# Kernel optimization log

Hardware: AMD Instinct MI355X
Metric: run time of the kernel (lower is better)

The kernel has to match this reference:

```python
import jax, jax.numpy as jnp
import numpy as np

N, FEAT, EMB, OUT = 16384, 256, 128, 128


def setup_inputs() -> dict:
    key = jax.random.key(0)
    k1, k2, k3, k4, k5 = jax.random.split(key, 5)
    s1 = 1.0 / np.sqrt(FEAT)
    s2 = 1.0 / np.sqrt(EMB)
    return {
        "x": jax.random.normal(k1, (N, FEAT), dtype=jnp.float32),
        "W1": jax.random.uniform(k2, (FEAT, EMB), jnp.float32, -s1, s1),
        "b1": jax.random.uniform(k3, (EMB,), jnp.float32, -s1, s1),
        "W2": jax.random.uniform(k4, (EMB, OUT), jnp.float32, -s2, s2),
        "b2": jax.random.uniform(k5, (OUT,), jnp.float32, -s2, s2),
    }


def reference(x, W1, b1, W2, b2):
    # projection: [N, feat] -> [N, emb]
    h = x @ W1 + b1
    # dense self-similarity graph: A_ = h h^T  (N x N)
    A_ = h @ h.T
    # degree-style normalization: A_ij -> 2*A_ij / (A_ii + A_jj)
    d = jnp.diagonal(A_)  # [N], == row squared norms of h
    A = 2.0 * A_ / (d[:, None] + d[None, :])
    # degree-normalized aggregation then output MLP + ReLU
    agg = A @ h  # [N, emb]
    return jax.nn.relu(agg @ W2 + b2)
```

## Files before the change

### kernel.cpp

```cpp
#include <hip/hip_runtime.h>
#include <stdint.h>

#define N_TOK 16384
#define FEAT  256
#define EMB   128
#define NQ    13
#define KC    16

typedef float  f32x4  __attribute__((ext_vector_type(4)));
typedef __bf16 bf16x8 __attribute__((ext_vector_type(8)));
typedef short  s16x8  __attribute__((ext_vector_type(8)));
typedef unsigned int u32x4 __attribute__((ext_vector_type(4)));

__device__ __forceinline__ unsigned short bf16_rne(float f) {
    union { float f; unsigned u; } v; v.f = f;
    unsigned u = v.u;
    return (unsigned short)((u + 0x7FFFu + ((u >> 16) & 1u)) >> 16);
}
__device__ __forceinline__ float bf16_to_f32(unsigned short s) {
    union { unsigned u; float f; } v; v.u = ((unsigned)s) << 16; return v.f;
}
__device__ __forceinline__ unsigned pack_trunc(float a, float b) {
    union { float f; unsigned u; } ua, ub; ua.f = a; ub.f = b;
    return (ub.u & 0xFFFF0000u) | (ua.u >> 16);
}
__device__ __forceinline__ void async_cp16(const void* g, void* l) {
    __builtin_amdgcn_global_load_lds(
        (const __attribute__((address_space(1))) unsigned int*)g,
        (__attribute__((address_space(3))) unsigned int*)l, 16, 0, 0);
}

__global__ void k0_transpose(const float* __restrict__ W1, const float* __restrict__ W2,
                             unsigned short* __restrict__ W1T, unsigned short* __restrict__ W2T)
{
    const int tid  = blockIdx.x * blockDim.x + threadIdx.x;
    const int nthr = gridDim.x * blockDim.x;
    for (int i = tid; i < FEAT * EMB; i += nthr) {
        const int r = i >> 7, c = i & 127;
        W1T[c * FEAT + r] = bf16_rne(W1[i]);
    }
    for (int i = tid; i < EMB * EMB; i += nthr) {
        const int r = i >> 7, c = i & 127;
        W2T[c * EMB + r] = bf16_rne(W2[i]);
    }
}

__global__ __launch_bounds__(256) void k1_proj(
    const float* __restrict__ x, const unsigned short* __restrict__ W1T,
    const float* __restrict__ b1,
    unsigned short* __restrict__ h, unsigned short* __restrict__ hT,
    float* __restrict__ UT)
{
    __shared__ __align__(16) unsigned char W1s[65536];
    __shared__ unsigned short ldsT[128 * 68];
    const int lane = threadIdx.x & 63;
    const int wave = threadIdx.x >> 6;
    const int quad = lane >> 4;
    const int l15  = lane & 15;
    const int arow = blockIdx.x * 64 + wave * 16 + l15;

    float4 xv[16];
    #pragma unroll
    for (int ks = 0; ks < 8; ++ks) {
        const float* xp = x + (size_t)arow * FEAT + ks * 32 + quad * 8;
        xv[2 * ks]     = *(const float4*)xp;
        xv[2 * ks + 1] = *(const float4*)(xp + 4);
    }
    #pragma unroll
    for (int c = 0; c < 16; ++c) {
        const int chunk = wave * 16 + c;
        const int row = chunk * 2 + (lane >> 5);
        const int b = (lane & 31) ^ (row & 15);
        async_cp16(W1T + (size_t)row * FEAT + b * 8, W1s + chunk * 1024);
    }
    bf16x8 afr[8];
    #pragma unroll
    for (int ks = 0; ks < 8; ++ks) {
        const float4 xa = xv[2 * ks], xb = xv[2 * ks + 1];
        s16x8 at;
        at[0] = (short)bf16_rne(xa.x); at[1] = (short)bf16_rne(xa.y);
        at[2] = (short)bf16_rne(xa.z); at[3] = (short)bf16_rne(xa.w);
        at[4] = (short)bf16_rne(xb.x); at[5] = (short)bf16_rne(xb.y);
        at[6] = (short)bf16_rne(xb.z); at[7] = (short)bf16_rne(xb.w);
        afr[ks] = __builtin_bit_cast(bf16x8, at);
    }
    __syncthreads();

    const f32x4 zero4 = {0.f, 0.f, 0.f, 0.f};
    f32x4 acc[8];
    #pragma unroll
    for (int n0 = 0; n0 < 8; ++n0) acc[n0] = zero4;
    #pragma unroll
    for (int ks = 0; ks < 8; ++ks)
        #pragma unroll
        for (int n0 = 0; n0 < 8; ++n0) {
            const int n = n0 * 16 + l15;
            const int b = (ks * 4 + quad) ^ (n & 15);
            const bf16x8 bfr = *(const bf16x8*)(W1s + n * 512 + b * 16);
            acc[n0] = __builtin_amdgcn_mfma_f32_16x16x32_bf16(afr[ks], bfr, acc[n0], 0, 0, 0);
        }

    const int rbase = blockIdx.x * 64 + wave * 16 + quad * 4;
    float dpart[4] = {0.f, 0.f, 0.f, 0.f};
    #pragma unroll
    for (int n0 = 0; n0 < 8; ++n0) {
        const int col = n0 * 16 + l15;
        const float bias = b1[col];
        unsigned short hb[4];
        #pragma unroll
        for (int r = 0; r < 4; ++r) {
            const float hv = acc[n0][r] + bias;
            const unsigned short q = bf16_rne(hv);
            hb[r] = q;
            const float bb = bf16_to_f32(q);
            dpart[r] += bb * bb;
            h[(size_t)(rbase + r) * EMB + col] = q;
        }
        ushort4 pk = make_ushort4(hb[0], hb[1], hb[2], hb[3]);
        *(ushort4*)&ldsT[col * 68 + wave * 16 + quad * 4] = pk;
    }
    const float tql = __expf(0.9f * (float)l15 - 10.8f);
    #pragma unroll
    for (int r = 0; r < 4; ++r) {
        float v = dpart[r];
        v += __shfl_xor(v, 1);
        v += __shfl_xor(v, 2);
        v += __shfl_xor(v, 4);
        v += __shfl_xor(v, 8);
        if (l15 < 12)       UT[(size_t)l15 * N_TOK + rbase + r] = __expf(-tql * v);
        else if (l15 == 12) UT[(size_t)12  * N_TOK + rbase + r] = 1.0f;
    }
    __syncthreads();
    const int rbase0 = blockIdx.x * 64;
    #pragma unroll
    for (int i = 0; i < 4; ++i) {
        const int slot = i * 256 + threadIdx.x;
        const int c    = slot >> 3;
        const int seg  = slot & 7;
        const ushort4 a0 = *(const ushort4*)&ldsT[c * 68 + seg * 8];
        const ushort4 a1 = *(const ushort4*)&ldsT[c * 68 + seg * 8 + 4];
        ushort4 o[2] = {a0, a1};
        *(uint4*)&hT[(size_t)c * N_TOK + rbase0 + seg * 8] = *(const uint4*)o;
    }
}

__global__ __launch_bounds__(256, 3) void k2a_gram(
    const unsigned short* __restrict__ hT, const float* __restrict__ UT,
    float* __restrict__ Gp)
{
    __shared__ __align__(16) unsigned char Rb[32768];
    const int lane = threadIdx.x & 63;
    const int wave = threadIdx.x >> 6;
    const int quad = lane >> 4;
    const int l15  = lane & 15;
    const int q  = blockIdx.x >> 4;
    const int kc = blockIdx.x & 15;
    const int E = wave & 1, F = wave >> 1;

    const f32x4 zero4 = {0.f, 0.f, 0.f, 0.f};
    f32x4 acc[4][4];
    #pragma unroll
    for (int mt = 0; mt < 4; ++mt)
        #pragma unroll
        for (int nt = 0; nt < 4; ++nt) acc[mt][nt] = zero4;

    #pragma unroll 1
    for (int sub = 0; sub < 8; ++sub) {
        const int kwin = kc * 1024 + sub * 128;
        __syncthreads();
        #pragma unroll
        for (int c = 0; c < 8; ++c) {
            const int chunk = wave * 8 + c;
            const int row = chunk * 4 + (lane >> 4);
            const int b = (lane & 15) ^ (row & 15);
            async_cp16(hT + (size_t)row * N_TOK + kwin + b * 8, Rb + chunk * 1024);
        }
        __syncthreads();

        #pragma unroll
        for (int ks = 0; ks < 4; ++ks) {
            const int kb = kwin + ks * 32 + quad * 8;
            const float4 ua = *(const float4*)(UT + (size_t)q * N_TOK + kb);
            const float4 ub = *(const float4*)(UT + (size_t)q * N_TOK + kb + 4);
            const float uv[8] = {ua.x, ua.y, ua.z, ua.w, ub.x, ub.y, ub.z, ub.w};
            bf16x8 au[4];
            #pragma unroll
            for (int mt = 0; mt < 4; ++mt) {
                const int re = E * 64 + mt * 16 + l15;
                const int b = (ks * 4 + quad) ^ (re & 15);
                const s16x8 raw = *(const s16x8*)(Rb + re * 256 + b * 16);
                u32x4 ww;
                #pragma unroll
                for (int w = 0; w < 4; ++w) {
                    const float fa = bf16_to_f32((unsigned short)raw[2 * w])     * uv[2 * w];
                    const float fb = bf16_to_f32((unsigned short)raw[2 * w + 1]) * uv[2 * w + 1];
                    ww[w] = pack_trunc(fa, fb);
                }
                au[mt] = __builtin_bit_cast(bf16x8, ww);
            }
            #pragma unroll
            for (int nt = 0; nt < 4; ++nt) {
                const int rf = F * 64 + nt * 16 + l15;
                const int b = (ks * 4 + quad) ^ (rf & 15);
                const bf16x8 bfr = *(const bf16x8*)(Rb + rf * 256 + b * 16);
                #pragma unroll
                for (int mt = 0; mt < 4; ++mt)
                    acc[mt][nt] = __builtin_amdgcn_mfma_f32_16x16x32_bf16(au[mt], bfr, acc[mt][nt], 0, 0, 0);
            }
        }
    }

    float* gp = Gp + (size_t)(q * KC + kc) * (EMB * EMB);
    #pragma unroll
    for (int mt = 0; mt < 4; ++mt)
        #pragma unroll
        for (int nt = 0; nt < 4; ++nt)
            #pragma unroll
            for (int r = 0; r < 4; ++r)
                gp[(size_t)(E * 64 + mt * 16 + quad * 4 + r) * EMB + F * 64 + nt * 16 + l15] = acc[mt][nt][r];
}

__global__ __launch_bounds__(256) void k2r_reduce(const float* __restrict__ Gp, float* __restrict__ G)
{
    const int q   = blockIdx.x >> 6;
    const int idx = (blockIdx.x & 63) * 256 + threadIdx.x;
    float s = 0.f;
    #pragma unroll
    for (int kc = 0; kc < KC; ++kc)
        s += Gp[(size_t)(q * KC + kc) * (EMB * EMB) + idx];
    G[(size_t)q * (EMB * EMB) + idx] = s;
}

__global__ __launch_bounds__(256) void k2b_gwt(
    const float* __restrict__ G, const unsigned short* __restrict__ W2T,
    unsigned short* __restrict__ GWT)
{
    const int q  = blockIdx.x >> 3;
    const int fs = blockIdx.x & 7;
    const int lane = threadIdx.x & 63;
    const int wave = threadIdx.x >> 6;
    const int quad = lane >> 4;
    const int l15  = lane & 15;
    const float scale = (q == 12) ? 2.0f * __expf(-10.8f)
                                  : 1.8f * __expf(0.9f * (float)q - 10.8f);
    const int fg = fs * 16 + l15;

    const f32x4 zero4 = {0.f, 0.f, 0.f, 0.f};
    f32x4 acc[2];
    acc[0] = zero4; acc[1] = zero4;
    #pragma unroll
    for (int ks = 0; ks < 4; ++ks) {
        const float* p = G + (size_t)q * (EMB * EMB) + (size_t)fg * EMB + ks * 32 + quad * 8;
        const float4 x1 = *(const float4*)p;
        const float4 x2 = *(const float4*)(p + 4);
        const float bv[8] = {x1.x, x1.y, x1.z, x1.w, x2.x, x2.y, x2.z, x2.w};
        s16x8 sb;
        #pragma unroll
        for (int j = 0; j < 8; ++j) sb[j] = (short)bf16_rne(bv[j]);
        const bf16x8 bfr = __builtin_bit_cast(bf16x8, sb);
        #pragma unroll
        for (int mt = 0; mt < 2; ++mt) {
            const int o = wave * 32 + mt * 16 + l15;
            const bf16x8 afr = *(const bf16x8*)(W2T + (size_t)o * EMB + ks * 32 + quad * 8);
            acc[mt] = __builtin_amdgcn_mfma_f32_16x16x32_bf16(afr, bfr, acc[mt], 0, 0, 0);
        }
    }
    #pragma unroll
    for (int mt = 0; mt < 2; ++mt)
        #pragma unroll
        for (int r = 0; r < 4; ++r)
            GWT[(size_t)q * (EMB * EMB) + (size_t)(wave * 32 + mt * 16 + quad * 4 + r) * EMB + fs * 16 + l15]
                = bf16_rne(acc[mt][r] * scale);
}

__global__ __launch_bounds__(256, 2) void k2c_apply(
    const unsigned short* __restrict__ h, const unsigned short* __restrict__ GWT,
    const float* __restrict__ UT, const float* __restrict__ b2,
    float* __restrict__ out)
{
    __shared__ __align__(16) unsigned char Gs[2][32768];
    const int lane = threadIdx.x & 63;
    const int wave = threadIdx.x >> 6;
    const int quad = lane >> 4;
    const int l15  = lane & 15;
    const int i0   = blockIdx.x * 32 + (wave & 1) * 16;
    const int F    = wave >> 1;
    const int irow = i0 + l15;

    bf16x8 araw[4];
    #pragma unroll
    for (int ks = 0; ks < 4; ++ks)
        araw[ks] = *(const bf16x8*)(h + (size_t)irow * EMB + ks * 32 + quad * 8);

    const f32x4 zero4 = {0.f, 0.f, 0.f, 0.f};
    f32x4 acc[4];
    #pragma unroll
    for (int nt = 0; nt < 4; ++nt) acc[nt] = zero4;

    #pragma unroll
    for (int c = 0; c < 8; ++c) {
        const int chunk = wave * 8 + c;
        const int row = chunk * 4 + (lane >> 4);
        const int b = (lane & 15) ^ (row & 15);
        async_cp16(GWT + (size_t)row * EMB + b * 8, &Gs[0][chunk * 1024]);
    }
    #pragma unroll 1
    for (int q = 0; q < NQ; ++q) {
        __syncthreads();
        if (q + 1 < NQ) {
            const unsigned short* src = GWT + (size_t)(q + 1) * (EMB * EMB);
            unsigned char* dst = Gs[(q + 1) & 1];
            #pragma unroll
            for (int c = 0; c < 8; ++c) {
                const int chunk = wave * 8 + c;
                const int row = chunk * 4 + (lane >> 4);
                const int b = (lane & 15) ^ (row & 15);
                async_cp16(src + (size_t)row * EMB + b * 8, dst + chunk * 1024);
            }
        }
        const float u = UT[(size_t)q * N_TOK + irow];
        bf16x8 au[4];
        #pragma unroll
        for (int ks = 0; ks < 4; ++ks) {
            const s16x8 raw = __builtin_bit_cast(s16x8, araw[ks]);
            u32x4 ww;
            #pragma unroll
            for (int w = 0; w < 4; ++w) {
                const float fa = bf16_to_f32((unsigned short)raw[2 * w])     * u;
                const float fb = bf16_to_f32((unsigned short)raw[2 * w + 1]) * u;
                ww[w] = pack_trunc(fa, fb);
            }
            au[ks] = __builtin_bit_cast(bf16x8, ww);
        }
        const unsigned char* gb = Gs[q & 1];
        #pragma unroll
        for (int nt = 0; nt < 4; ++nt) {
            const int o = F * 64 + nt * 16 + l15;
            #pragma unroll
            for (int ks = 0; ks < 4; ++ks) {
                const int b = (ks * 4 + quad) ^ (o & 15);
                const bf16x8 bfr = *(const bf16x8*)(gb + o * 256 + b * 16);
                acc[nt] = __builtin_amdgcn_mfma_f32_16x16x32_bf16(au[ks], bfr, acc[nt], 0, 0, 0);
            }
        }
    }

    #pragma unroll
    for (int nt = 0; nt < 4; ++nt) {
        const int o = F * 64 + nt * 16 + l15;
        const float bias = b2[o];
        #pragma unroll
        for (int r = 0; r < 4; ++r) {
            const float v = acc[nt][r] + bias;
            out[(size_t)(i0 + quad * 4 + r) * EMB + o] = v > 0.f ? v : 0.f;
        }
    }
}

extern "C" void kernel_launch(void* const* d_in, const int* in_sizes, int n_in,
                              void* d_out, int out_size, void* d_ws, size_t ws_size,
                              hipStream_t stream) {
    const float* x  = (const float*)d_in[0];
    const float* W1 = (const float*)d_in[1];
    const float* b1 = (const float*)d_in[2];
    const float* W2 = (const float*)d_in[3];
    const float* b2 = (const float*)d_in[4];
    float* out = (float*)d_out;

    char* ws = (char*)d_ws;
    unsigned short* h   = (unsigned short*)(ws);
    unsigned short* hT  = (unsigned short*)(ws + 4194304);
    unsigned short* W1T = (unsigned short*)(ws + 8388608);
    unsigned short* W2T = (unsigned short*)(ws + 8454144);
    float*          UT  = (float*)        (ws + 8486912);
    float*          Gp  = (float*)        (ws + 9338880);
    float*          G   = (float*)        (ws + 23068672);
    unsigned short* GWT = (unsigned short*)(ws + 23920640);

    k0_transpose<<<dim3(16),      dim3(256), 0, stream>>>(W1, W2, W1T, W2T);
    k1_proj     <<<dim3(256),     dim3(256), 0, stream>>>(x, W1T, b1, h, hT, UT);
    k2a_gram    <<<dim3(NQ * KC), dim3(256), 0, stream>>>(hT, UT, Gp);
    k2r_reduce  <<<dim3(NQ * 64), dim3(256), 0, stream>>>(Gp, G);
    k2b_gwt     <<<dim3(NQ * 8),  dim3(256), 0, stream>>>(G, W2T, GWT);
    k2c_apply   <<<dim3(512),     dim3(256), 0, stream>>>(h, GWT, UT, b2, out);
}
```

Before: 134.5 us.

## Fuse weight transpose and partial-Gram reduction into consumers, widen apply tiles

Removes the separate W1/W2 transpose kernel by having k1_proj convert and swizzle W1 into LDS directly, and k2b_gwt read W2 with strided loads. Removes the k2r_reduce kernel by summing the KC partial Gram matrices inside k2b_gwt. k2c_apply now handles 64 rows per block with two row groups sharing each LDS B-fragment, which halves the grid. The bf16 truncation pack uses a byte-permute intrinsic. Fewer launches and less intermediate traffic come at the cost of redundant per-block W1 conversion and strided, uncoalesced W2 reads.

```diff
diff --git a/kernel.cpp b/kernel.cpp
--- a/kernel.cpp
+++ b/kernel.cpp
@@ -20,9 +20,9 @@
 __device__ __forceinline__ float bf16_to_f32(unsigned short s) {
     union { unsigned u; float f; } v; v.u = ((unsigned)s) << 16; return v.f;
 }
-__device__ __forceinline__ unsigned pack_trunc(float a, float b) {
+__device__ __forceinline__ unsigned pack_perm(float a, float b) {
     union { float f; unsigned u; } ua, ub; ua.f = a; ub.f = b;
-    return (ub.u & 0xFFFF0000u) | (ua.u >> 16);
+    return __builtin_amdgcn_perm(ub.u, ua.u, 0x07060302u);
 }
 __device__ __forceinline__ void async_cp16(const void* g, void* l) {
     __builtin_amdgcn_global_load_lds(
@@ -30,23 +30,8 @@
         (__attribute__((address_space(3))) unsigned int*)l, 16, 0, 0);
 }
 
-__global__ void k0_transpose(const float* __restrict__ W1, const float* __restrict__ W2,
-                             unsigned short* __restrict__ W1T, unsigned short* __restrict__ W2T)
-{
-    const int tid  = blockIdx.x * blockDim.x + threadIdx.x;
-    const int nthr = gridDim.x * blockDim.x;
-    for (int i = tid; i < FEAT * EMB; i += nthr) {
-        const int r = i >> 7, c = i & 127;
-        W1T[c * FEAT + r] = bf16_rne(W1[i]);
-    }
-    for (int i = tid; i < EMB * EMB; i += nthr) {
-        const int r = i >> 7, c = i & 127;
-        W2T[c * EMB + r] = bf16_rne(W2[i]);
-    }
-}
-
 __global__ __launch_bounds__(256) void k1_proj(
-    const float* __restrict__ x, const unsigned short* __restrict__ W1T,
+    const float* __restrict__ x, const float* __restrict__ W1,
     const float* __restrict__ b1,
     unsigned short* __restrict__ h, unsigned short* __restrict__ hT,
     float* __restrict__ UT)
@@ -66,12 +51,25 @@
         xv[2 * ks]     = *(const float4*)xp;
         xv[2 * ks + 1] = *(const float4*)(xp + 4);
     }
-    #pragma unroll
-    for (int c = 0; c < 16; ++c) {
-        const int chunk = wave * 16 + c;
-        const int row = chunk * 2 + (lane >> 5);
-        const int b = (lane & 31) ^ (row & 15);
-        async_cp16(W1T + (size_t)row * FEAT + b * 8, W1s + chunk * 1024);
+    {
+        const int c0 = (threadIdx.x & 31) * 4;
+        #pragma unroll
+        for (int i = 0; i < 8; ++i) {
+            const int k0 = ((threadIdx.x >> 5) + i * 8) * 4;
+            float4 row[4];
+            #pragma unroll
+            for (int j = 0; j < 4; ++j)
+                row[j] = *(const float4*)(W1 + (size_t)(k0 + j) * EMB + c0);
+            #pragma unroll
+            for (int j2 = 0; j2 < 4; ++j2) {
+                const int c = c0 + j2;
+                ushort4 pk = make_ushort4(
+                    bf16_rne((&row[0].x)[j2]), bf16_rne((&row[1].x)[j2]),
+                    bf16_rne((&row[2].x)[j2]), bf16_rne((&row[3].x)[j2]));
+                const int blk = (k0 >> 3) ^ (c & 15);
+                *(ushort4*)(W1s + c * 512 + blk * 16 + (k0 & 7) * 2) = pk;
+            }
+        }
     }
     bf16x8 afr[8];
     #pragma unroll
@@ -194,7 +192,7 @@
                 for (int w = 0; w < 4; ++w) {
                     const float fa = bf16_to_f32((unsigned short)raw[2 * w])     * uv[2 * w];
                     const float fb = bf16_to_f32((unsigned short)raw[2 * w + 1]) * uv[2 * w + 1];
-                    ww[w] = pack_trunc(fa, fb);
+                    ww[w] = pack_perm(fa, fb);
                 }
                 au[mt] = __builtin_bit_cast(bf16x8, ww);
             }
@@ -220,19 +218,8 @@
                 gp[(size_t)(E * 64 + mt * 16 + quad * 4 + r) * EMB + F * 64 + nt * 16 + l15] = acc[mt][nt][r];
 }
 
-__global__ __launch_bounds__(256) void k2r_reduce(const float* __restrict__ Gp, float* __restrict__ G)
-{
-    const int q   = blockIdx.x >> 6;
-    const int idx = (blockIdx.x & 63) * 256 + threadIdx.x;
-    float s = 0.f;
-    #pragma unroll
-    for (int kc = 0; kc < KC; ++kc)
-        s += Gp[(size_t)(q * KC + kc) * (EMB * EMB) + idx];
-    G[(size_t)q * (EMB * EMB) + idx] = s;
-}
-
 __global__ __launch_bounds__(256) void k2b_gwt(
-    const float* __restrict__ G, const unsigned short* __restrict__ W2T,
+    const float* __restrict__ Gp, const float* __restrict__ W2,
     unsigned short* __restrict__ GWT)
 {
     const int q  = blockIdx.x >> 3;
@@ -250,10 +237,15 @@
     acc[0] = zero4; acc[1] = zero4;
     #pragma unroll
     for (int ks = 0; ks < 4; ++ks) {
-        const float* p = G + (size_t)q * (EMB * EMB) + (size_t)fg * EMB + ks * 32 + quad * 8;
-        const float4 x1 = *(const float4*)p;
-        const float4 x2 = *(const float4*)(p + 4);
-        const float bv[8] = {x1.x, x1.y, x1.z, x1.w, x2.x, x2.y, x2.z, x2.w};
+        float bv[8] = {0,0,0,0,0,0,0,0};
+        #pragma unroll
+        for (int kc = 0; kc < KC; ++kc) {
+            const float* p = Gp + (size_t)(q * KC + kc) * (EMB * EMB) + (size_t)fg * EMB + ks * 32 + quad * 8;
+            const float4 x1 = *(const float4*)p;
+            const float4 x2 = *(const float4*)(p + 4);
+            bv[0] += x1.x; bv[1] += x1.y; bv[2] += x1.z; bv[3] += x1.w;
+            bv[4] += x2.x; bv[5] += x2.y; bv[6] += x2.z; bv[7] += x2.w;
+        }
         s16x8 sb;
         #pragma unroll
         for (int j = 0; j < 8; ++j) sb[j] = (short)bf16_rne(bv[j]);
@@ -261,7 +253,11 @@
         #pragma unroll
         for (int mt = 0; mt < 2; ++mt) {
             const int o = wave * 32 + mt * 16 + l15;
-            const bf16x8 afr = *(const bf16x8*)(W2T + (size_t)o * EMB + ks * 32 + quad * 8);
+            s16x8 aw;
+            #pragma unroll
+            for (int j = 0; j < 8; ++j)
+                aw[j] = (short)bf16_rne(W2[(size_t)(ks * 32 + quad * 8 + j) * EMB + o]);
+            const bf16x8 afr = __builtin_bit_cast(bf16x8, aw);
             acc[mt] = __builtin_amdgcn_mfma_f32_16x16x32_bf16(afr, bfr, acc[mt], 0, 0, 0);
         }
     }
@@ -283,19 +279,22 @@
     const int wave = threadIdx.x >> 6;
     const int quad = lane >> 4;
     const int l15  = lane & 15;
-    const int i0   = blockIdx.x * 32 + (wave & 1) * 16;
+    const int i0   = blockIdx.x * 64 + (wave & 1) * 32;
     const int F    = wave >> 1;
-    const int irow = i0 + l15;
-
-    bf16x8 araw[4];
-    #pragma unroll
-    for (int ks = 0; ks < 4; ++ks)
-        araw[ks] = *(const bf16x8*)(h + (size_t)irow * EMB + ks * 32 + quad * 8);
+
+    bf16x8 araw[2][4];
+    #pragma unroll
+    for (int g = 0; g < 2; ++g)
+        #pragma unroll
+        for (int ks = 0; ks < 4; ++ks)
+            araw[g][ks] = *(const bf16x8*)(h + (size_t)(i0 + g * 16 + l15) * EMB + ks * 32 + quad * 8);
 
     const f32x4 zero4 = {0.f, 0.f, 0.f, 0.f};
-    f32x4 acc[4];
-    #pragma unroll
-    for (int nt = 0; nt < 4; ++nt) acc[nt] = zero4;
+    f32x4 acc[2][4];
+    #pragma unroll
+    for (int g = 0; g < 2; ++g)
+        #pragma unroll
+        for (int nt = 0; nt < 4; ++nt) acc[g][nt] = zero4;
 
     #pragma unroll
     for (int c = 0; c < 8; ++c) {
@@ -318,19 +317,22 @@
                 async_cp16(src + (size_t)row * EMB + b * 8, dst + chunk * 1024);
             }
         }
-        const float u = UT[(size_t)q * N_TOK + irow];
-        bf16x8 au[4];
-        #pragma unroll
-        for (int ks = 0; ks < 4; ++ks) {
-            const s16x8 raw = __builtin_bit_cast(s16x8, araw[ks]);
-            u32x4 ww;
-            #pragma unroll
-            for (int w = 0; w < 4; ++w) {
-                const float fa = bf16_to_f32((unsigned short)raw[2 * w])     * u;
-                const float fb = bf16_to_f32((unsigned short)raw[2 * w + 1]) * u;
-                ww[w] = pack_trunc(fa, fb);
-            }
-            au[ks] = __builtin_bit_cast(bf16x8, ww);
+        bf16x8 au[2][4];
+        #pragma unroll
+        for (int g = 0; g < 2; ++g) {
+            const float u = UT[(size_t)q * N_TOK + i0 + g * 16 + l15];
+            #pragma unroll
+            for (int ks = 0; ks < 4; ++ks) {
+                const s16x8 raw = __builtin_bit_cast(s16x8, araw[g][ks]);
+                u32x4 ww;
+                #pragma unroll
+                for (int w = 0; w < 4; ++w) {
+                    const float fa = bf16_to_f32((unsigned short)raw[2 * w])     * u;
+                    const float fb = bf16_to_f32((unsigned short)raw[2 * w + 1]) * u;
+                    ww[w] = pack_perm(fa, fb);
+                }
+                au[g][ks] = __builtin_bit_cast(bf16x8, ww);
+            }
         }
         const unsigned char* gb = Gs[q & 1];
         #pragma unroll
@@ -340,21 +342,25 @@
             for (int ks = 0; ks < 4; ++ks) {
                 const int b = (ks * 4 + quad) ^ (o & 15);
                 const bf16x8 bfr = *(const bf16x8*)(gb + o * 256 + b * 16);
-                acc[nt] = __builtin_amdgcn_mfma_f32_16x16x32_bf16(au[ks], bfr, acc[nt], 0, 0, 0);
-            }
-        }
-    }
-
-    #pragma unroll
-    for (int nt = 0; nt < 4; ++nt) {
-        const int o = F * 64 + nt * 16 + l15;
-        const float bias = b2[o];
-        #pragma unroll
-        for (int r = 0; r < 4; ++r) {
-            const float v = acc[nt][r] + bias;
-            out[(size_t)(i0 + quad * 4 + r) * EMB + o] = v > 0.f ? v : 0.f;
-        }
-    }
+                #pragma unroll
+                for (int g = 0; g < 2; ++g)
+                    acc[g][nt] = __builtin_amdgcn_mfma_f32_16x16x32_bf16(au[g][ks], bfr, acc[g][nt], 0, 0, 0);
+            }
+        }
+    }
+
+    #pragma unroll
+    for (int g = 0; g < 2; ++g)
+        #pragma unroll
+        for (int nt = 0; nt < 4; ++nt) {
+            const int o = F * 64 + nt * 16 + l15;
+            const float bias = b2[o];
+            #pragma unroll
+            for (int r = 0; r < 4; ++r) {
+                const float v = acc[g][nt][r] + bias;
+                out[(size_t)(i0 + g * 16 + quad * 4 + r) * EMB + o] = v > 0.f ? v : 0.f;
+            }
+        }
 }
 
 extern "C" void kernel_launch(void* const* d_in, const int* in_sizes, int n_in,
@@ -370,17 +376,12 @@
     char* ws = (char*)d_ws;
     unsigned short* h   = (unsigned short*)(ws);
     unsigned short* hT  = (unsigned short*)(ws + 4194304);
-    unsigned short* W1T = (unsigned short*)(ws + 8388608);
-    unsigned short* W2T = (unsigned short*)(ws + 8454144);
-    float*          UT  = (float*)        (ws + 8486912);
-    float*          Gp  = (float*)        (ws + 9338880);
-    float*          G   = (float*)        (ws + 23068672);
-    unsigned short* GWT = (unsigned short*)(ws + 23920640);
-
-    k0_transpose<<<dim3(16),      dim3(256), 0, stream>>>(W1, W2, W1T, W2T);
-    k1_proj     <<<dim3(256),     dim3(256), 0, stream>>>(x, W1T, b1, h, hT, UT);
-    k2a_gram    <<<dim3(NQ * KC), dim3(256), 0, stream>>>(hT, UT, Gp);
-    k2r_reduce  <<<dim3(NQ * 64), dim3(256), 0, stream>>>(Gp, G);
-    k2b_gwt     <<<dim3(NQ * 8),  dim3(256), 0, stream>>>(G, W2T, GWT);
-    k2c_apply   <<<dim3(512),     dim3(256), 0, stream>>>(h, GWT, UT, b2, out);
-}
+    float*          UT  = (float*)        (ws + 8388608);
+    float*          Gp  = (float*)        (ws + 9240576);
+    unsigned short* GWT = (unsigned short*)(ws + 22872064);
+
+    k1_proj  <<<dim3(256),     dim3(256), 0, stream>>>(x, W1, b1, h, hT, UT);
+    k2a_gram <<<dim3(NQ * KC), dim3(256), 0, stream>>>(hT, UT, Gp);
+    k2b_gwt  <<<dim3(NQ * 8),  dim3(256), 0, stream>>>(Gp, W2, GWT);
+    k2c_apply<<<dim3(256),     dim3(256), 0, stream>>>(h, GWT, UT, b2, out);
+}
```

New measurement: 141.4 us. 5.2% more time.
